# Kernel optimization log

Hardware: AMD Instinct MI355X
Metric: run time of the kernel (lower is better)

The kernel has to match this reference:

```python
import jax, jax.numpy as jnp
import numpy as np

IMAGE_SIZE = 320
SIGMA = 0.01      # soft-edge width in NDC units (~1.6 px at 320 res)
CHUNK = 128       # faces per scan step (bounds peak memory)


def setup_inputs() -> dict:
    key = jax.random.key(0)
    k1, k2 = jax.random.split(key)
    verts = jax.random.normal(k1, (4, 778, 3), dtype=jnp.float32) * 0.5
    faces = jax.random.randint(k2, (1538, 3), 0, 778, dtype=jnp.int32)
    return {"verts": verts, "faces": faces}


def _silhouette(verts, faces):
    B = verts.shape[0]
    S = IMAGE_SIZE
    # NMR.forward flips the y axis of verts before rendering
    v = verts * jnp.array([1.0, -1.0, 1.0], dtype=verts.dtype)
    xy = v[..., :2]  # orthographic projection (perspective=False)
    F = faces.shape[0]
    n_chunks = -(-F // CHUNK)
    Fp = n_chunks * CHUNK
    faces_p = jnp.pad(faces, ((0, Fp - F), (0, 0)))
    valid = (jnp.arange(Fp) < F).astype(verts.dtype)
    tri = xy[:, faces_p]  # [B, Fp, 3, 2]
    tri = jnp.moveaxis(tri.reshape(B, n_chunks, CHUNK, 3, 2), 1, 0)  # [nc,B,C,3,2]
    valid = valid.reshape(n_chunks, CHUNK)
    # pixel centers in NDC [-1, 1]
    lin = (jnp.arange(S, dtype=verts.dtype) + 0.5) / S * 2.0 - 1.0
    py, px = jnp.meshgrid(lin, lin, indexing="ij")
    px = px.reshape(-1)  # [P]
    py = py.reshape(-1)

    def edge_d(a, b, sgn):
        # signed distance of every pixel to oriented edge a->b: [B, C, P]
        ex = b[..., 0] - a[..., 0]
        ey = b[..., 1] - a[..., 1]
        inv_len = 1.0 / (jnp.sqrt(ex * ex + ey * ey) + 1e-8)
        d = (ex[..., None] * (py[None, None, :] - a[..., 1:2])
             - ey[..., None] * (px[None, None, :] - a[..., 0:1]))
        return sgn[..., None] * d * inv_len[..., None]

    def body(acc, chunk):
        tri_c, m = chunk  # [B,C,3,2], [C]
        v0, v1, v2 = tri_c[..., 0, :], tri_c[..., 1, :], tri_c[..., 2, :]
        # orientation sign so CW / CCW triangles are handled uniformly
        area2 = ((v1[..., 0] - v0[..., 0]) * (v2[..., 1] - v0[..., 1])
                 - (v1[..., 1] - v0[..., 1]) * (v2[..., 0] - v0[..., 0]))
        sgn = jnp.sign(area2)
        logp = (jax.nn.log_sigmoid(edge_d(v0, v1, sgn) / SIGMA)
                + jax.nn.log_sigmoid(edge_d(v1, v2, sgn) / SIGMA)
                + jax.nn.log_sigmoid(edge_d(v2, v0, sgn) / SIGMA))
        prob = jnp.clip(jnp.exp(logp) * m[None, :, None], 0.0, 1.0 - 1e-6)
        return acc + jnp.sum(jnp.log1p(-prob), axis=1), None

    acc0 = jnp.zeros((B, S * S), dtype=verts.dtype)
    acc, _ = jax.lax.scan(body, acc0, (tri, valid))
    # silhouette = 1 - prod_f (1 - coverage_f), accumulated in log space
    return (1.0 - jnp.exp(acc)).reshape(B, S, S)


def reference(verts, faces):
    return _silhouette(verts, faces)
```

## Files before the change

kernel.cpp:

```cpp
#include <hip/hip_runtime.h>
#include <math.h>


#define IMG_S 320
#define N_FACES 1538
#define N_VERTS 778
#define N_BATCH 4
#define FP 1600
#define TILE 8
#define CHUNK_F 256
#define NWAVE 4
#define INV_SIGMA 100.0f
#define T_CUT 14.0f
#define ACC_CUT_P 2.0611536e-9f
#define LOG2_1EM6 -19.9315686f

__global__ __launch_bounds__(256)
void prep_faces(const float* __restrict__ verts,
                const int* __restrict__ faces,
                float4* __restrict__ gE0,
                float4* __restrict__ gE1,
                float4* __restrict__ gE2)
{
    const int f = blockIdx.x * 256 + threadIdx.x;
    const int b = blockIdx.z;
    if (f >= N_FACES) return;

    const float* vb = verts + (size_t)b * N_VERTS * 3;
    const int i0 = faces[f * 3 + 0];
    const int i1 = faces[f * 3 + 1];
    const int i2 = faces[f * 3 + 2];
    const float x0 = vb[i0 * 3 + 0], y0 = -vb[i0 * 3 + 1];
    const float x1 = vb[i1 * 3 + 0], y1 = -vb[i1 * 3 + 1];
    const float x2 = vb[i2 * 3 + 0], y2 = -vb[i2 * 3 + 1];

    const float dx1 = x1 - x0, dy1 = y1 - y0;
    const float dx2 = x2 - x0, dy2 = y2 - y0;
    const float area2 = __builtin_fmaf(dx1, dy2, -__fmul_rn(dy1, dx2));
    const float sgn = (area2 > 0.0f) ? 1.0f : ((area2 < 0.0f) ? -1.0f : 0.0f);

    const size_t o = (size_t)b * FP + f;
    {
        const float ex = x1 - x0, ey = y1 - y0;
        const float s = sgn * INV_SIGMA / (sqrtf(ex * ex + ey * ey) + 1e-8f);
        gE0[o] = make_float4(-s * ey, s * ex, s * (ey * x0 - ex * y0), 0.0f);
    }
    {
        const float ex = x2 - x1, ey = y2 - y1;
        const float s = sgn * INV_SIGMA / (sqrtf(ex * ex + ey * ey) + 1e-8f);
        gE1[o] = make_float4(-s * ey, s * ex, s * (ey * x1 - ex * y1), 0.0f);
    }
    {
        const float ex = x0 - x2, ey = y0 - y2;
        const float s = sgn * INV_SIGMA / (sqrtf(ex * ex + ey * ey) + 1e-8f);
        gE2[o] = make_float4(-s * ey, s * ex, s * (ey * x2 - ex * y2), 0.0f);
    }
}

__global__ __launch_bounds__(256)
void silhouette_ws(const float4* __restrict__ gE0,
                   const float4* __restrict__ gE1,
                   const float4* __restrict__ gE2,
                   float* __restrict__ out)
{
    __shared__ float4 sE0[CHUNK_F];
    __shared__ float4 sE1[CHUNK_F];
    __shared__ float4 sE2[CHUNK_F];
    __shared__ float sAcc[256];
    __shared__ int sCount;
    __shared__ int sAlive;
    __shared__ int sCover;

    const int t    = threadIdx.x;
    const int wave = t >> 6;
    const int p    = t & 63;
    const int b    = blockIdx.z;
    const int lx   = p & 7;
    const int ly   = p >> 3;
    const int gx   = blockIdx.x * TILE + lx;
    const int gy   = blockIdx.y * TILE + ly;

    const float w  = 2.0f / IMG_S;
    const float px = (gx + 0.5f) * w - 1.0f;
    const float py = (gy + 0.5f) * w - 1.0f;
    const float cx = (blockIdx.x * TILE + 4) * w - 1.0f;
    const float cy = (blockIdx.y * TILE + 4) * w - 1.0f;
    const float rr = 3.5f * w;

    float acc = 1.0f;

    const int nchunks = (N_FACES + CHUNK_F - 1) / CHUNK_F;
    for (int c = 0; c < nchunks; ++c) {
        sAcc[t] = acc;
        if (t == 0) { sCount = 0; sAlive = 0; sCover = 0; }
        __syncthreads();

        const float tot = sAcc[p] * sAcc[p + 64] * sAcc[p + 128] * sAcc[p + 192];
        const bool alive = (tot > ACC_CUT_P);
        if (alive) sAlive = 1;

        const int fc = c * CHUNK_F + t;
        if (fc < N_FACES) {
            const size_t o = (size_t)b * FP + fc;
            const float4 e0 = gE0[o];
            const float4 e1 = gE1[o];
            const float4 e2 = gE2[o];
            const float c0 = fmaf(e0.x, cx, fmaf(e0.y, cy, e0.z));
            const float c1 = fmaf(e1.x, cx, fmaf(e1.y, cy, e1.z));
            const float c2 = fmaf(e2.x, cx, fmaf(e2.y, cy, e2.z));
            const float r0 = rr * (fabsf(e0.x) + fabsf(e0.y));
            const float r1 = rr * (fabsf(e1.x) + fabsf(e1.y));
            const float r2 = rr * (fabsf(e2.x) + fabsf(e2.y));
            const float m_hi = fminf(c0 + r0, fminf(c1 + r1, c2 + r2));
            const float m_lo = fminf(c0 - r0, fminf(c1 - r1, c2 - r2));
            if (m_lo > T_CUT) {
                atomicAdd(&sCover, 1);
            } else if (m_hi > -T_CUT) {
                const int slot = atomicAdd(&sCount, 1);
                sE0[slot] = e0;
                sE1[slot] = e1;
                sE2[slot] = e2;
            }
        }
        __syncthreads();

        if (sAlive == 0) break;

        const float coverF = exp2f((float)sCover * LOG2_1EM6);
        bool live = alive && (acc * coverF > ACC_CUT_P);
        if (wave == 0) acc *= coverF;

        const int n = sCount;
        for (int j = wave; j < n; j += NWAVE) {
            if (__ballot(live) == 0ull) break;
            const float4 e0 = sE0[j];
            const float4 e1 = sE1[j];
            const float4 e2 = sE2[j];
            const float xa = fmaf(e0.x, px, fmaf(e0.y, py, e0.z));
            const float xb = fmaf(e1.x, px, fmaf(e1.y, py, e1.z));
            const float xc = fmaf(e2.x, px, fmaf(e2.y, py, e2.z));
            const float m = fminf(xa, fminf(xb, xc));
            if (live && m > -T_CUT) {
                if (m > T_CUT) {
                    acc *= 1e-6f;
                } else {
                    const float mid = fmaxf(fminf(fmaxf(xa, xb), xc),
                                            fminf(xa, xb));
                    float f;
                    if (mid > T_CUT) {
                        f = __builtin_amdgcn_rcpf(1.0f + __expf(m));
                    } else {
                        const float da = 1.0f + __expf(-xa);
                        const float db = 1.0f + __expf(-xb);
                        const float dc = 1.0f + __expf(-xc);
                        f = 1.0f - __builtin_amdgcn_rcpf(da * db * dc);
                    }
                    acc *= fmaxf(f, 1e-6f);
                }
                live = (acc > ACC_CUT_P);
            }
        }

        __syncthreads();
    }

    sAcc[t] = acc;
    __syncthreads();
    if (t < 64) {
        const float tot = sAcc[p] * sAcc[p + 64] * sAcc[p + 128] * sAcc[p + 192];
        out[(size_t)b * (IMG_S * IMG_S) + (size_t)gy * IMG_S + gx] = 1.0f - tot;
    }
}

extern "C" void kernel_launch(void* const* d_in, const int* in_sizes, int n_in,
                              void* d_out, int out_size, void* d_ws, size_t ws_size,
                              hipStream_t stream) {
    const float* verts = (const float*)d_in[0];
    const int* faces = (const int*)d_in[1];
    float* out = (float*)d_out;

    float4* gE0 = (float4*)d_ws;
    float4* gE1 = gE0 + (size_t)N_BATCH * FP;
    float4* gE2 = gE1 + (size_t)N_BATCH * FP;

    dim3 pgrid((N_FACES + 255) / 256, 1, N_BATCH);
    prep_faces<<<pgrid, 256, 0, stream>>>(verts, faces, gE0, gE1, gE2);

    dim3 grid(IMG_S / TILE, IMG_S / TILE, N_BATCH);
    silhouette_ws<<<grid, 256, 0, stream>>>(gE0, gE1, gE2, out);
}
```

Baseline: 92.08 us.

## Bin faces by index with wave ballots, loosen cutoffs, use two chunks

Face binning now uses one ballot and one LDS atomic per wave instead of per-thread atomics, and stores only face indices in shared memory. The inner loop reloads edge coefficients from global memory through a wave-uniform index. Chunking changes to two passes (768 faces, then the rest). The saturation and early-exit thresholds are loosened (T_CUT 14→12, ACC_CUT_P ~2e-9→~2e-6), which lets more work be skipped but lowers the accuracy of coverage values near 1.

```diff
diff --git a/kernel.cpp b/kernel.cpp
--- a/kernel.cpp
+++ b/kernel.cpp
@@ -8,11 +8,11 @@
 #define N_BATCH 4
 #define FP 1600
 #define TILE 8
-#define CHUNK_F 256
+#define CHUNK_F 768
 #define NWAVE 4
 #define INV_SIGMA 100.0f
-#define T_CUT 14.0f
-#define ACC_CUT_P 2.0611536e-9f
+#define T_CUT 12.0f
+#define ACC_CUT_P 2.2603294e-6f
 #define LOG2_1EM6 -19.9315686f
 
 __global__ __launch_bounds__(256)
@@ -63,9 +63,7 @@
                    const float4* __restrict__ gE2,
                    float* __restrict__ out)
 {
-    __shared__ float4 sE0[CHUNK_F];
-    __shared__ float4 sE1[CHUNK_F];
-    __shared__ float4 sE2[CHUNK_F];
+    __shared__ int sIdx[CHUNK_F + 8];
     __shared__ float sAcc[256];
     __shared__ int sCount;
     __shared__ int sAlive;
@@ -73,12 +71,13 @@
 
     const int t    = threadIdx.x;
     const int wave = t >> 6;
+    const int lane = t & 63;
     const int p    = t & 63;
+    const int plx  = p & 7;
+    const int ply  = p >> 3;
     const int b    = blockIdx.z;
-    const int lx   = p & 7;
-    const int ly   = p >> 3;
-    const int gx   = blockIdx.x * TILE + lx;
-    const int gy   = blockIdx.y * TILE + ly;
+    const int gx   = blockIdx.x * TILE + plx;
+    const int gy   = blockIdx.y * TILE + ply;
 
     const float w  = 2.0f / IMG_S;
     const float px = (gx + 0.5f) * w - 1.0f;
@@ -87,10 +86,16 @@
     const float cy = (blockIdx.y * TILE + 4) * w - 1.0f;
     const float rr = 3.5f * w;
 
+    const float4* gb0 = gE0 + (size_t)b * FP;
+    const float4* gb1 = gE1 + (size_t)b * FP;
+    const float4* gb2 = gE2 + (size_t)b * FP;
+
     float acc = 1.0f;
 
-    const int nchunks = (N_FACES + CHUNK_F - 1) / CHUNK_F;
-    for (int c = 0; c < nchunks; ++c) {
+    for (int c = 0; c < 2; ++c) {
+        const int base = c * CHUNK_F;
+        const int end  = (c == 0) ? CHUNK_F : N_FACES;
+
         sAcc[t] = acc;
         if (t == 0) { sCount = 0; sAlive = 0; sCover = 0; }
         __syncthreads();
@@ -98,13 +103,17 @@
         const float tot = sAcc[p] * sAcc[p + 64] * sAcc[p + 128] * sAcc[p + 192];
         const bool alive = (tot > ACC_CUT_P);
         if (alive) sAlive = 1;
-
-        const int fc = c * CHUNK_F + t;
-        if (fc < N_FACES) {
-            const size_t o = (size_t)b * FP + fc;
-            const float4 e0 = gE0[o];
-            const float4 e1 = gE1[o];
-            const float4 e2 = gE2[o];
+        __syncthreads();
+
+        if (sAlive == 0) break;
+
+        for (int fb = base; fb < end; fb += 256) {
+            const int fc = fb + t;
+            const bool vald = (fc < end);
+            const int fcc = vald ? fc : (end - 1);
+            const float4 e0 = gb0[fcc];
+            const float4 e1 = gb1[fcc];
+            const float4 e2 = gb2[fcc];
             const float c0 = fmaf(e0.x, cx, fmaf(e0.y, cy, e0.z));
             const float c1 = fmaf(e1.x, cx, fmaf(e1.y, cy, e1.z));
             const float c2 = fmaf(e2.x, cx, fmaf(e2.y, cy, e2.z));
@@ -113,18 +122,26 @@
             const float r2 = rr * (fabsf(e2.x) + fabsf(e2.y));
             const float m_hi = fminf(c0 + r0, fminf(c1 + r1, c2 + r2));
             const float m_lo = fminf(c0 - r0, fminf(c1 - r1, c2 - r2));
-            if (m_lo > T_CUT) {
-                atomicAdd(&sCover, 1);
-            } else if (m_hi > -T_CUT) {
-                const int slot = atomicAdd(&sCount, 1);
-                sE0[slot] = e0;
-                sE1[slot] = e1;
-                sE2[slot] = e2;
+            const bool isCov  = vald && (m_lo > T_CUT);
+            const bool isBand = vald && !isCov && (m_hi > -T_CUT);
+
+            const unsigned long long mb = __ballot(isBand);
+            int wbase = 0;
+            if (lane == 0) {
+                const int nw = __popcll(mb);
+                if (nw) wbase = atomicAdd(&sCount, nw);
+            }
+            wbase = __shfl(wbase, 0);
+            if (isBand) {
+                sIdx[wbase + __popcll(mb & ((1ull << lane) - 1ull))] = fc;
+            }
+            const unsigned long long mc = __ballot(isCov);
+            if (lane == 0) {
+                const int ncv = __popcll(mc);
+                if (ncv) atomicAdd(&sCover, ncv);
             }
         }
         __syncthreads();
-
-        if (sAlive == 0) break;
 
         const float coverF = exp2f((float)sCover * LOG2_1EM6);
         bool live = alive && (acc * coverF > ACC_CUT_P);
@@ -133,30 +150,33 @@
         const int n = sCount;
         for (int j = wave; j < n; j += NWAVE) {
             if (__ballot(live) == 0ull) break;
-            const float4 e0 = sE0[j];
-            const float4 e1 = sE1[j];
-            const float4 e2 = sE2[j];
+            int fj = sIdx[j];
+            fj = __builtin_amdgcn_readfirstlane(fj);
+            const float4 e0 = gb0[fj];
+            const float4 e1 = gb1[fj];
+            const float4 e2 = gb2[fj];
             const float xa = fmaf(e0.x, px, fmaf(e0.y, py, e0.z));
             const float xb = fmaf(e1.x, px, fmaf(e1.y, py, e1.z));
             const float xc = fmaf(e2.x, px, fmaf(e2.y, py, e2.z));
             const float m = fminf(xa, fminf(xb, xc));
             if (live && m > -T_CUT) {
+                float f;
                 if (m > T_CUT) {
-                    acc *= 1e-6f;
+                    f = 1e-6f;
                 } else {
                     const float mid = fmaxf(fminf(fmaxf(xa, xb), xc),
                                             fminf(xa, xb));
-                    float f;
                     if (mid > T_CUT) {
-                        f = __builtin_amdgcn_rcpf(1.0f + __expf(m));
+                        f = 1.0f - __builtin_amdgcn_rcpf(1.0f + __expf(-m));
                     } else {
                         const float da = 1.0f + __expf(-xa);
                         const float db = 1.0f + __expf(-xb);
                         const float dc = 1.0f + __expf(-xc);
                         f = 1.0f - __builtin_amdgcn_rcpf(da * db * dc);
                     }
-                    acc *= fmaxf(f, 1e-6f);
+                    f = fmaxf(f, 1e-6f);
                 }
+                acc *= f;
                 live = (acc > ACC_CUT_P);
             }
         }
```

Measured after the change: 87.96 us. -4.5%, faster.
